# Kernel optimization log

Hardware: AMD Instinct MI355X
Metric: run time of the kernel (lower is better)

The kernel has to match this reference:

```python
import jax, jax.numpy as jnp
import numpy as np

EMA_DECAY = 0.99


def setup_inputs() -> dict:
    key = jax.random.key(0)
    k1, k2, k3 = jax.random.split(key, 3)
    B, T, D, K = 32, 8192, 64, 512
    x = jax.random.normal(k1, (B, T, D), dtype=jnp.float32)
    embedding = jax.random.normal(k2, (K, D), dtype=jnp.float32)
    count = jnp.ones((K,), dtype=jnp.float32)
    sum_embed = jax.random.normal(k3, (K, D), dtype=jnp.float32)
    return {"x": x, "embedding": embedding, "count": count, "sum_embed": sum_embed}


def reference(x, embedding, count, sum_embed):
    # is_training=True path of Quantizer.call
    K, D = embedding.shape
    flat = x.reshape(-1, D)  # [N, D]
    N = flat.shape[0]
    dist = (
        jnp.sum(flat * flat, axis=1, keepdims=True)
        - 2.0 * flat @ embedding.T
        + jnp.sum(embedding * embedding, axis=1)
    )
    encoding_index = jnp.argmin(dist, axis=1)  # [N]

    # one-hot counts and sums expressed as segment sums (avoids [K, N] onehot)
    c = jax.ops.segment_sum(jnp.ones((N,), dtype=jnp.float32), encoding_index, num_segments=K)
    new_sum = jax.ops.segment_sum(flat, encoding_index, num_segments=K)  # [K, D]

    count = count + (1.0 - EMA_DECAY) * (c - count)
    usage = (count >= 1.0).astype(jnp.float32)  # [K]
    count = count * usage + (1.0 - usage)
    sum_embed = sum_embed + (1.0 - EMA_DECAY) * (new_sum - sum_embed)

    # re-seed dead codes with random input vectors
    r = jax.random.randint(jax.random.key(1), (K,), 0, N)
    usage2 = usage[:, None]
    embedding_new = usage2 * (sum_embed / count[:, None]) + (1.0 - usage2) * flat[r]

    quantized = embedding_new[encoding_index].reshape(x.shape)
    # straight-through estimator
    quantized = x + jax.lax.stop_gradient(quantized - x)
    return quantized
```

## Files before the change

### kernel.cpp

```cpp
#include <hip/hip_runtime.h>

#define D 64
#define KC 512
#define EMA_A 0.01f
#define SCHUNK 1024
#define NCHUNK 256
#define HROWS 1024
#define NHB 256
#define BAND 0.0078125f

typedef float f32x4 __attribute__((ext_vector_type(4)));
typedef float v4f __attribute__((ext_vector_type(4)));
typedef short s8v __attribute__((ext_vector_type(8)));
typedef short s4v __attribute__((ext_vector_type(4)));

__device__ inline unsigned short bf16_rne(float f) {
    unsigned u = __float_as_uint(f);
    return (unsigned short)((u + 0x7fffu + ((u >> 16) & 1u)) >> 16);
}
__device__ inline float bf16_f(unsigned short h) {
    return __uint_as_float(((unsigned)h) << 16);
}

__global__ __launch_bounds__(256) void k_prep(const float* __restrict__ emb,
                                              float* __restrict__ he,
                                              short* __restrict__ gB,
                                              int* __restrict__ wcount) {
    if (blockIdx.x == 0 && threadIdx.x == 0) wcount[0] = 0;
    int k = blockIdx.x * 256 + threadIdx.x;
    if (k >= KC) return;
    int c8 = k >> 6, c = k & 63;
    short* dst = gB + (size_t)c8 * 8192;
    float s = 0.f;
#pragma unroll
    for (int kq = 0; kq < 16; ++kq) {
        float4 v = ((const float4*)(emb + (size_t)k * D))[kq];
        s = fmaf(v.x, v.x, s); s = fmaf(v.y, v.y, s);
        s = fmaf(v.z, v.z, s); s = fmaf(v.w, v.w, s);
        unsigned short h0 = bf16_rne(v.x), h1 = bf16_rne(v.y);
        unsigned short h2 = bf16_rne(v.z), h3 = bf16_rne(v.w);
        s4v hv = {(short)h0, (short)h1, (short)h2, (short)h3};
        s4v lv = {(short)bf16_rne(v.x - bf16_f(h0)),
                  (short)bf16_rne(v.y - bf16_f(h1)),
                  (short)bf16_rne(v.z - bf16_f(h2)),
                  (short)bf16_rne(v.w - bf16_f(h3))};
        int si = c * 64 + (((kq >> 1) ^ (c & 7)) * 8) + (kq & 1) * 4;
        *(s4v*)(&dst[si]) = hv;
        *(s4v*)(&dst[4096 + si]) = lv;
    }
    he[k] = 0.5f * s;
}

__global__ __launch_bounds__(256, 4) void k_assign(
    const float* __restrict__ x, const short* __restrict__ gB,
    const float* __restrict__ he, int* __restrict__ idx,
    int* __restrict__ wlist, int* __restrict__ wcount) {
    __shared__ __align__(16) short LB[2][8192];
    __shared__ int wl_cnt, wl_base;
    __shared__ int wl_rows[128];
    int tid = threadIdx.x;
    int lane = tid & 63, w = tid >> 6, q = lane >> 4, c16 = lane & 15;
    size_t R0 = (size_t)blockIdx.x * 128;
    if (tid == 0) wl_cnt = 0;

    const float4* xg = (const float4*)(x + R0 * D);
#pragma unroll
    for (int p = 0; p < 8; ++p) {
        int flat = p * 256 + tid;
        int row = flat >> 4, kq = flat & 15;
        float4 v = xg[flat];
        unsigned short h0 = bf16_rne(v.x), h1 = bf16_rne(v.y);
        unsigned short h2 = bf16_rne(v.z), h3 = bf16_rne(v.w);
        s4v hv = {(short)h0, (short)h1, (short)h2, (short)h3};
        s4v lv = {(short)bf16_rne(v.x - bf16_f(h0)),
                  (short)bf16_rne(v.y - bf16_f(h1)),
                  (short)bf16_rne(v.z - bf16_f(h2)),
                  (short)bf16_rne(v.w - bf16_f(h3))};
        int si = row * 64 + (((kq >> 1) ^ (row & 7)) * 8) + (kq & 1) * 4;
        *(s4v*)(&LB[0][si]) = hv;
        *(s4v*)(&LB[1][si]) = lv;
    }
    __syncthreads();

    s8v ah[2][2], al[2][2];
#pragma unroll
    for (int rt = 0; rt < 2; ++rt)
#pragma unroll
        for (int ks = 0; ks < 2; ++ks) {
            int row = w * 32 + rt * 16 + c16;
            int kb = (ks * 4 + q) ^ (row & 7);
            ah[rt][ks] = *(const s8v*)(&LB[0][row * 64 + kb * 8]);
            al[rt][ks] = *(const s8v*)(&LB[1][row * 64 + kb * 8]);
        }
    __syncthreads();

#pragma unroll
    for (int p = 0; p < 4; ++p)
        ((int4*)LB[0])[p * 256 + tid] = ((const int4*)gB)[p * 256 + tid];
    __syncthreads();

    float m1[8], m2[8]; int i1[8];
#pragma unroll
    for (int e = 0; e < 8; ++e) { m1[e] = 3.4e38f; m2[e] = 3.4e38f; i1[e] = 0; }

    for (int c8 = 0; c8 < 8; ++c8) {
        if (c8 < 7) {
            const int4* src = (const int4*)(gB + (size_t)(c8 + 1) * 8192);
            int4* dst = (int4*)LB[(c8 + 1) & 1];
#pragma unroll
            for (int p = 0; p < 4; ++p)
                dst[p * 256 + tid] = src[p * 256 + tid];
        }
        const short* LBc = LB[c8 & 1];
#pragma unroll
        for (int ct = 0; ct < 4; ++ct) {
            s8v bh[2], bl[2];
#pragma unroll
            for (int ks = 0; ks < 2; ++ks) {
                int c = ct * 16 + c16;
                int kb = (ks * 4 + q) ^ (c & 7);
                bh[ks] = *(const s8v*)(&LBc[c * 64 + kb * 8]);
                bl[ks] = *(const s8v*)(&LBc[4096 + c * 64 + kb * 8]);
            }
            int cbase = c8 * 64 + ct * 16;
            float hec = he[cbase + c16];
            int ci = cbase + c16;
#pragma unroll
            for (int rt = 0; rt < 2; ++rt) {
                f32x4 acc = {0.f, 0.f, 0.f, 0.f};
                acc = __builtin_amdgcn_mfma_f32_16x16x32_bf16(ah[rt][0], bh[0], acc, 0, 0, 0);
                acc = __builtin_amdgcn_mfma_f32_16x16x32_bf16(ah[rt][1], bh[1], acc, 0, 0, 0);
                acc = __builtin_amdgcn_mfma_f32_16x16x32_bf16(ah[rt][0], bl[0], acc, 0, 0, 0);
                acc = __builtin_amdgcn_mfma_f32_16x16x32_bf16(ah[rt][1], bl[1], acc, 0, 0, 0);
                acc = __builtin_amdgcn_mfma_f32_16x16x32_bf16(al[rt][0], bh[0], acc, 0, 0, 0);
                acc = __builtin_amdgcn_mfma_f32_16x16x32_bf16(al[rt][1], bh[1], acc, 0, 0, 0);
                acc = __builtin_amdgcn_mfma_f32_16x16x32_bf16(al[rt][0], bl[0], acc, 0, 0, 0);
                acc = __builtin_amdgcn_mfma_f32_16x16x32_bf16(al[rt][1], bl[1], acc, 0, 0, 0);
#pragma unroll
                for (int r = 0; r < 4; ++r) {
                    float d = hec - acc[r];
                    int e = rt * 4 + r;
                    m2[e] = fminf(m2[e], fmaxf(d, m1[e]));
                    bool lt = d < m1[e];
                    i1[e] = lt ? ci : i1[e];
                    m1[e] = fminf(m1[e], d);
                }
            }
        }
        __syncthreads();
    }
#pragma unroll
    for (int m = 1; m < 16; m <<= 1) {
#pragma unroll
        for (int e = 0; e < 8; ++e) {
            float om1 = __shfl_xor(m1[e], m);
            float om2 = __shfl_xor(m2[e], m);
            int oi = __shfl_xor(i1[e], m);
            float nm2 = fminf(fminf(m2[e], om2), fmaxf(m1[e], om1));
            bool take = (om1 < m1[e]) || (om1 == m1[e] && oi < i1[e]);
            i1[e] = take ? oi : i1[e];
            m1[e] = fminf(m1[e], om1);
            m2[e] = nm2;
        }
    }
    if (c16 == 0) {
#pragma unroll
        for (int e = 0; e < 8; ++e) {
            int row = (int)R0 + w * 32 + (e >> 2) * 16 + q * 4 + (e & 3);
            idx[row] = i1[e];
            if (m2[e] - m1[e] < BAND) {
                int p = atomicAdd(&wl_cnt, 1);
                wl_rows[p] = row;
            }
        }
    }
    __syncthreads();
    if (tid == 0 && wl_cnt > 0) wl_base = atomicAdd(wcount, wl_cnt);
    __syncthreads();
    for (int i = tid; i < wl_cnt; i += 256) wlist[wl_base + i] = wl_rows[i];
}

__global__ __launch_bounds__(256) void k_recheck(
    const float* __restrict__ x, const float* __restrict__ emb,
    const float* __restrict__ he, const int* __restrict__ wlist,
    const int* __restrict__ wcount, int* __restrict__ idx) {
    int lane = threadIdx.x & 63;
    int wave = (blockIdx.x * 256 + threadIdx.x) >> 6;
    int nwaves = (gridDim.x * 256) >> 6;
    int cnt = wcount[0];
    for (int i = wave; i < cnt; i += nwaves) {
        int row = wlist[i];
        const v4f* xr = (const v4f*)(x + (size_t)row * D);
        v4f X[16];
#pragma unroll
        for (int t = 0; t < 16; ++t) X[t] = xr[t];
        float bd = 3.4e38f; int bi = 0x7fffffff;
#pragma unroll
        for (int j = 0; j < 8; ++j) {
            int c = j * 64 + lane;
            const v4f* er = (const v4f*)(emb + (size_t)c * D);
            v4f s = X[0] * er[0];
#pragma unroll
            for (int t = 1; t < 16; ++t) s += X[t] * er[t];
            float dot = (s.x + s.y) + (s.z + s.w);
            float d = he[c] - dot;
            if (d < bd) { bd = d; bi = c; }
        }
#pragma unroll
        for (int m = 1; m < 64; m <<= 1) {
            float od = __shfl_xor(bd, m);
            int oi = __shfl_xor(bi, m);
            if (od < bd || (od == bd && oi < bi)) { bd = od; bi = oi; }
        }
        if (lane == 0) idx[row] = bi;
    }
}

__global__ __launch_bounds__(256) void k_hist(const int* __restrict__ idx,
                                              float* __restrict__ gcount) {
    __shared__ int hist[KC];
    int tid = threadIdx.x;
    for (int i = tid; i < KC; i += 256) hist[i] = 0;
    __syncthreads();
    int base = blockIdx.x * HROWS;
    for (int r = base + tid; r < base + HROWS; r += 256)
        atomicAdd(&hist[idx[r]], 1);
    __syncthreads();
    for (int i = tid; i < KC; i += 256)
        gcount[(size_t)blockIdx.x * KC + i] = (float)hist[i];
}

__global__ __launch_bounds__(512) void k_segsum(
    const float* __restrict__ x, const int* __restrict__ idx,
    float* __restrict__ gpart, int N) {
    __shared__ float part[256 * D];
    int tid = threadIdx.x;
    int chunk = blockIdx.x >> 1;
    int half = blockIdx.x & 1;
    int base = chunk * SCHUNK;
    int end = base + SCHUNK; if (end > N) end = N;
    for (int i = tid; i < 256 * D; i += 512) part[i] = 0.f;
    __syncthreads();
    for (int r = base + tid; r < end; r += 512) {
        int k = idx[r];
        if ((k >> 8) == half) {
            int kl = k & 255;
            const float4* p = (const float4*)(x + (size_t)r * D);
#pragma unroll
            for (int i = 0; i < D / 4; ++i) {
                float4 v = p[i];
                int d = 4 * i;
                atomicAdd(&part[kl * D + ((d + 0 + kl) & 63)], v.x);
                atomicAdd(&part[kl * D + ((d + 1 + kl) & 63)], v.y);
                atomicAdd(&part[kl * D + ((d + 2 + kl) & 63)], v.z);
                atomicAdd(&part[kl * D + ((d + 3 + kl) & 63)], v.w);
            }
        }
    }
    __syncthreads();
    size_t ob = (size_t)chunk * (KC * D) + (size_t)half * (256 * D);
    for (int i = tid; i < 256 * D; i += 512) {
        int kl = i >> 6, d = i & 63;
        gpart[ob + i] = part[kl * D + ((d + kl) & 63)];
    }
}

__global__ __launch_bounds__(256) void k_final(
    const float* __restrict__ gpart, const float* __restrict__ gcount,
    const float* __restrict__ cnt_in, const float* __restrict__ sum_embed,
    float* __restrict__ embnew) {
    __shared__ float cs[4];
    int tid = threadIdx.x;
    int i = blockIdx.x * 256 + tid;
    float s = 0.f;
#pragma unroll 4
    for (int c = 0; c < NCHUNK; ++c) s += gpart[(size_t)c * (KC * D) + i];
    if ((tid & 63) == 0) {
        int k = i >> 6;
        float c = 0.f;
#pragma unroll 4
        for (int b = 0; b < NHB; ++b) c += gcount[(size_t)b * KC + k];
        cs[tid >> 6] = c;
    }
    __syncthreads();
    float c = cs[tid >> 6];
    float c0 = cnt_in[i >> 6];
    float cn = c0 + EMA_A * (c - c0);
    float se0 = sum_embed[i];
    float se = se0 + EMA_A * (s - se0);
    embnew[i] = (cn >= 1.0f) ? (se / cn) : 0.0f;
}

__global__ __launch_bounds__(256) void k_gather(const int* __restrict__ idx,
                                                const float* __restrict__ embnew,
                                                float* __restrict__ out, int N) {
    int g = blockIdx.x * 256 + threadIdx.x;
    int row = g >> 4, q = g & 15;
    if (row >= N) return;
    int k = idx[row];
    const float4* e4 = (const float4*)embnew;
    ((float4*)out)[(size_t)row * (D / 4) + q] = e4[k * (D / 4) + q];
}

extern "C" void kernel_launch(void* const* d_in, const int* in_sizes, int n_in,
                              void* d_out, int out_size, void* d_ws, size_t ws_size,
                              hipStream_t stream) {
    const float* x = (const float*)d_in[0];
    const float* emb = (const float*)d_in[1];
    const float* cnt = (const float*)d_in[2];
    const float* sum_embed = (const float*)d_in[3];
    float* out = (float*)d_out;
    int N = in_sizes[0] / D;

    char* w = (char*)d_ws;
    size_t off = 0;
    int* idx = (int*)(w + off);        off += (size_t)N * 4;
    int* wlist = (int*)(w + off);      off += (size_t)N * 4;
    int* wcount = (int*)(w + off);     off += 16;
    float* he = (float*)(w + off);     off += (size_t)KC * 4;
    short* gB = (short*)(w + off);     off += (size_t)8 * 8192 * 2;
    float* embnew = (float*)(w + off); off += (size_t)KC * D * 4;
    float* gcount = (float*)(w + off); off += (size_t)NHB * KC * 4;
    float* gpart = (float*)(w + off);  off += (size_t)NCHUNK * KC * D * 4;

    k_prep<<<(KC + 255) / 256, 256, 0, stream>>>(emb, he, gB, wcount);
    k_assign<<<N / 128, 256, 0, stream>>>(x, gB, he, idx, wlist, wcount);
    k_recheck<<<512, 256, 0, stream>>>(x, emb, he, wlist, wcount, idx);
    k_hist<<<NHB, 256, 0, stream>>>(idx, gcount);
    k_segsum<<<NCHUNK * 2, 512, 0, stream>>>(x, idx, gpart, N);
    k_final<<<(KC * D) / 256, 256, 0, stream>>>(gpart, gcount, cnt, sum_embed, embnew);
    k_gather<<<((size_t)N * (D / 4)) / 256, 256, 0, stream>>>(idx, embnew, out, N);
}
```

Baseline: 363.9 us.

## Compute segment sums as one-hot matrix multiply on MFMA with bf16 hi/lo split

Replaces the LDS-atomic segment sum with a one-hot times x product on MFMA matrix cores. Each block builds one-hot A fragments from the indices and splits x into bf16 high and low parts, running two MFMAs per tile to keep near-fp32 accuracy. Each block now covers all 512 codes for its 1024 rows, so the grid drops from 512 to 256 blocks. This removes contended shared-memory float atomics, at the cost of doing dense work over all codes and dropping the low-order bits that fall outside the bf16 split.

```diff
diff --git a/kernel.cpp b/kernel.cpp
--- a/kernel.cpp
+++ b/kernel.cpp
@@ -3,7 +3,7 @@
 #define D 64
 #define KC 512
 #define EMA_A 0.01f
-#define SCHUNK 1024
+#define SROWS 1024
 #define NCHUNK 256
 #define HROWS 1024
 #define NHB 256
@@ -230,39 +230,75 @@
         gcount[(size_t)blockIdx.x * KC + i] = (float)hist[i];
 }
 
-__global__ __launch_bounds__(512) void k_segsum(
+__global__ __launch_bounds__(512, 1) void k_segsum(
     const float* __restrict__ x, const int* __restrict__ idx,
-    float* __restrict__ gpart, int N) {
-    __shared__ float part[256 * D];
+    float* __restrict__ gpart) {
+    __shared__ int sidx[SROWS];
+    __shared__ unsigned xpk[32 * 64];
     int tid = threadIdx.x;
-    int chunk = blockIdx.x >> 1;
-    int half = blockIdx.x & 1;
-    int base = chunk * SCHUNK;
-    int end = base + SCHUNK; if (end > N) end = N;
-    for (int i = tid; i < 256 * D; i += 512) part[i] = 0.f;
-    __syncthreads();
-    for (int r = base + tid; r < end; r += 512) {
-        int k = idx[r];
-        if ((k >> 8) == half) {
-            int kl = k & 255;
-            const float4* p = (const float4*)(x + (size_t)r * D);
-#pragma unroll
-            for (int i = 0; i < D / 4; ++i) {
-                float4 v = p[i];
-                int d = 4 * i;
-                atomicAdd(&part[kl * D + ((d + 0 + kl) & 63)], v.x);
-                atomicAdd(&part[kl * D + ((d + 1 + kl) & 63)], v.y);
-                atomicAdd(&part[kl * D + ((d + 2 + kl) & 63)], v.z);
-                atomicAdd(&part[kl * D + ((d + 3 + kl) & 63)], v.w);
-            }
-        }
-    }
-    __syncthreads();
-    size_t ob = (size_t)chunk * (KC * D) + (size_t)half * (256 * D);
-    for (int i = tid; i < 256 * D; i += 512) {
-        int kl = i >> 6, d = i & 63;
-        gpart[ob + i] = part[kl * D + ((d + kl) & 63)];
-    }
+    int lane = tid & 63, w = tid >> 6, q = lane >> 4, c16 = lane & 15;
+    int nb0 = blockIdx.x * SROWS;
+    for (int i = tid; i < SROWS; i += 512) sidx[i] = idx[nb0 + i];
+
+    f32x4 acc[4][4];
+#pragma unroll
+    for (int a = 0; a < 4; ++a)
+#pragma unroll
+        for (int b = 0; b < 4; ++b) acc[a][b] = (f32x4){0.f, 0.f, 0.f, 0.f};
+
+    int row32 = tid >> 4, d4 = tid & 15;
+    for (int ch = 0; ch < SROWS / 32; ++ch) {
+        __syncthreads();
+        float4 v = ((const float4*)(x + (size_t)(nb0 + ch * 32 + row32) * D))[d4];
+        float vals[4] = {v.x, v.y, v.z, v.w};
+#pragma unroll
+        for (int i = 0; i < 4; ++i) {
+            unsigned short h = bf16_rne(vals[i]);
+            unsigned short l = bf16_rne(vals[i] - bf16_f(h));
+            int d = d4 * 4 + i;
+            xpk[row32 * 64 + ((d + 2 * row32) & 63)] =
+                (unsigned)h | ((unsigned)l << 16);
+        }
+        __syncthreads();
+
+        int iv[8];
+#pragma unroll
+        for (int j = 0; j < 8; ++j) iv[j] = sidx[ch * 32 + q * 8 + j];
+        s8v af[4];
+#pragma unroll
+        for (int kt = 0; kt < 4; ++kt) {
+            int tgt = w * 64 + kt * 16 + c16;
+#pragma unroll
+            for (int j = 0; j < 8; ++j)
+                af[kt][j] = (iv[j] == tgt) ? (short)0x3F80 : (short)0;
+        }
+#pragma unroll
+        for (int dt = 0; dt < 4; ++dt) {
+            s8v bh, bl;
+#pragma unroll
+            for (int j = 0; j < 8; ++j) {
+                int n32 = q * 8 + j;
+                unsigned pv = xpk[n32 * 64 + ((dt * 16 + c16 + 2 * n32) & 63)];
+                bh[j] = (short)(pv & 0xffff);
+                bl[j] = (short)(pv >> 16);
+            }
+#pragma unroll
+            for (int kt = 0; kt < 4; ++kt) {
+                acc[kt][dt] = __builtin_amdgcn_mfma_f32_16x16x32_bf16(af[kt], bh, acc[kt][dt], 0, 0, 0);
+                acc[kt][dt] = __builtin_amdgcn_mfma_f32_16x16x32_bf16(af[kt], bl, acc[kt][dt], 0, 0, 0);
+            }
+        }
+    }
+    float* gp = gpart + (size_t)blockIdx.x * (KC * D);
+#pragma unroll
+    for (int kt = 0; kt < 4; ++kt)
+#pragma unroll
+        for (int dt = 0; dt < 4; ++dt)
+#pragma unroll
+            for (int r = 0; r < 4; ++r) {
+                int k = w * 64 + kt * 16 + q * 4 + r;
+                gp[k * D + dt * 16 + c16] = acc[kt][dt][r];
+            }
 }
 
 __global__ __launch_bounds__(256) void k_final(
@@ -327,7 +363,7 @@
     k_assign<<<N / 128, 256, 0, stream>>>(x, gB, he, idx, wlist, wcount);
     k_recheck<<<512, 256, 0, stream>>>(x, emb, he, wlist, wcount, idx);
     k_hist<<<NHB, 256, 0, stream>>>(idx, gcount);
-    k_segsum<<<NCHUNK * 2, 512, 0, stream>>>(x, idx, gpart, N);
+    k_segsum<<<NCHUNK, 512, 0, stream>>>(x, idx, gpart);
     k_final<<<(KC * D) / 256, 256, 0, stream>>>(gpart, gcount, cnt, sum_embed, embnew);
     k_gather<<<((size_t)N * (D / 4)) / 256, 256, 0, stream>>>(idx, embnew, out, N);
 }
```

After: 321.1 us. 1.13x faster.
